# Kernel optimization log

Measured on AMD Instinct MI355X. Metric: run time of the kernel, lower is better.

Reference implementation:

```python
import jax, jax.numpy as jnp
import numpy as np

ROPE_BASE = 10000.0

def _rope_cos_sin(T, d, dtype):
    inv_freq = 1.0 / (ROPE_BASE ** (jnp.arange(0, d, 2, dtype=jnp.float32) / d))
    t = jnp.arange(T, dtype=jnp.float32)
    freqs = t[:, None] * inv_freq[None, :]           # [T, d/2]
    emb = jnp.concatenate([freqs, freqs], axis=-1)   # [T, d]
    return jnp.cos(emb).astype(dtype), jnp.sin(emb).astype(dtype)

def _rotate_half(x):
    x1, x2 = jnp.split(x, 2, axis=-1)
    return jnp.concatenate([-x2, x1], axis=-1)

def setup_inputs() -> dict:
    key = jax.random.key(0)
    k1, k2, k3, k4 = jax.random.split(key, 4)
    B, T, C, H = 4, 4096, 1024, 64
    x = jax.random.normal(k1, (B, T, C), dtype=jnp.float32)
    s = 1.0 / np.sqrt(C)
    Wq = jax.random.normal(k2, (H, C), dtype=jnp.float32) * s
    Wk = jax.random.normal(k3, (H, C), dtype=jnp.float32) * s
    Wv = jax.random.normal(k4, (H, C), dtype=jnp.float32) * s
    return {"x": x, "Wq": Wq, "Wk": Wk, "Wv": Wv}

def reference(x, Wq, Wk, Wv):
    B, T, C = x.shape
    H = Wq.shape[0]
    q = jnp.einsum('btc,hc->bth', x, Wq)
    k = jnp.einsum('btc,hc->bth', x, Wk)
    v = jnp.einsum('btc,hc->bth', x, Wv)
    cos, sin = _rope_cos_sin(T, H, x.dtype)
    q = q * cos + _rotate_half(q) * sin
    k = k * cos + _rotate_half(k) * sin
    # NOTE: original scales by dim_model**-0.5 (C), not head_size
    wei = jnp.einsum('bth,bsh->bts', q, k) * (C ** -0.5)
    causal = jnp.tril(jnp.ones((T, T), dtype=bool))
    wei = jnp.where(causal, wei, -jnp.inf)
    wei = jax.nn.softmax(wei, axis=-1)
    # dropout p=0.0 (identity)
    out = jnp.einsum('bts,bsh->bth', wei, v)
    return out
```

## Files before the change

### kernel.cpp

```cpp
#include <hip/hip_runtime.h>
#include <hip/hip_bf16.h>
#include <math.h>

typedef __attribute__((ext_vector_type(8))) __bf16 bf16x8;
typedef __attribute__((ext_vector_type(4))) float f32x4;
typedef __attribute__((ext_vector_type(16))) float f32x16;
typedef __attribute__((ext_vector_type(4))) float float4_t;
typedef __attribute__((ext_vector_type(4))) unsigned int uint4_t;

#define NB 4
#define TSEQ 4096
#define CD 1024
#define HD 64
#define NCH 32
#define CHT 2

static __device__ __forceinline__ unsigned short f2bf(float f) {
    union { float f; unsigned u; } v; v.f = f;
    unsigned r = v.u + 0x7fffu + ((v.u >> 16) & 1u);
    return (unsigned short)(r >> 16);
}
static __device__ __forceinline__ float bf2f(unsigned short u) {
    union { unsigned int i; float f; } v; v.i = ((unsigned int)u) << 16;
    return v.f;
}
static __device__ __forceinline__ unsigned int pk2(float a, float b) {
    union { __bf16 h[2]; unsigned int u; } x;
    x.h[0] = (__bf16)a; x.h[1] = (__bf16)b;
    return x.u;
}

__global__ __launch_bounds__(256) void wcvt_kernel(const float* __restrict__ wq,
                                                   const float* __restrict__ wk,
                                                   const float* __restrict__ wv,
                                                   unsigned short* __restrict__ wb) {
    int i = blockIdx.x * 256 + threadIdx.x;
    int j = i >> 10;
    int col = i & 1023;
    int jb = j >> 4, off = j & 15;
    int sub = ((jb & 1) << 5) | ((jb & 2) << 3);
    int srcrow = (jb < 8) ? (sub + off) : ((jb - 8) * 16 + off);
    const float* src = (jb < 4) ? wq : ((jb < 8) ? wk : wv);
    wb[i] = f2bf(src[srcrow * 1024 + col]);
}

__global__ __launch_bounds__(256) void qkv_kernel(const float* __restrict__ x,
                                                  const unsigned short* __restrict__ wb,
                                                  unsigned short* __restrict__ qo,
                                                  unsigned short* __restrict__ ko,
                                                  unsigned short* __restrict__ vt) {
    __shared__ unsigned short xs[64][72];
    __shared__ unsigned short ws[64][72];
    const int tid = threadIdx.x;
    const int wave = tid >> 6, lane = tid & 63;
    const int lr = lane & 15;
    const int lk = (lane >> 4) << 3;
    const int rowg = (lane >> 4) << 2;
    const int row0 = blockIdx.x * 64;
    const int cbi = blockIdx.y;
    const int cb = cbi * 64;

    f32x4 acc[4];
#pragma unroll
    for (int i = 0; i < 4; ++i) acc[i] = (f32x4){0.f, 0.f, 0.f, 0.f};

    const int sr = tid >> 2;
    const int sc = (tid & 3) << 4;

    for (int k0 = 0; k0 < CD; k0 += 64) {
        __syncthreads();
        {
            const float4_t* s4 =
                reinterpret_cast<const float4_t*>(x + (size_t)(row0 + sr) * CD + k0 + sc);
            alignas(16) unsigned short tmp[16];
#pragma unroll
            for (int j = 0; j < 4; ++j) {
                float4_t f = s4[j];
#pragma unroll
                for (int e = 0; e < 4; ++e) tmp[j * 4 + e] = f2bf(f[e]);
            }
            *reinterpret_cast<uint4_t*>(&xs[sr][sc]) = *reinterpret_cast<const uint4_t*>(&tmp[0]);
            *reinterpret_cast<uint4_t*>(&xs[sr][sc + 8]) = *reinterpret_cast<const uint4_t*>(&tmp[8]);
        }
        {
            const uint4_t* wsrc =
                reinterpret_cast<const uint4_t*>(wb + (size_t)(cb + sr) * CD + k0 + sc);
            *reinterpret_cast<uint4_t*>(&ws[sr][sc]) = wsrc[0];
            *reinterpret_cast<uint4_t*>(&ws[sr][sc + 8]) = wsrc[1];
        }
        __syncthreads();
#pragma unroll
        for (int kk = 0; kk < 2; ++kk) {
            bf16x8 a = *reinterpret_cast<const bf16x8*>(&xs[wave * 16 + lr][kk * 32 + lk]);
#pragma unroll
            for (int c = 0; c < 4; ++c) {
                bf16x8 bfr = *reinterpret_cast<const bf16x8*>(&ws[c * 16 + lr][kk * 32 + lk]);
                acc[c] = __builtin_amdgcn_mfma_f32_16x16x32_bf16(a, bfr, acc[c], 0, 0, 0);
            }
        }
    }

    const int gr0 = row0 + wave * 16 + rowg;
    const int bidx = gr0 >> 12;
    const int tb = gr0 & (TSEQ - 1);
    if (cbi < 2) {
        unsigned short* o = (cbi == 0) ? qo : ko;
        const float sc2 = (cbi == 0) ? 0.045084218764560315f : 1.0f;
        const float l2b = 0.4152410118609215f;
        const float invf0 = exp2f(-(float)lr * l2b);
        const float invf1 = exp2f(-(float)(lr + 16) * l2b);
#pragma unroll
        for (int r = 0; r < 4; ++r) {
            float t = (float)(tb + r);
            float s0, c0, s1, c1;
            sincosf(t * invf0, &s0, &c0);
            sincosf(t * invf1, &s1, &c1);
            size_t ro = (size_t)(gr0 + r) * HD;
            float lo, hi;
            lo = acc[0][r]; hi = acc[1][r];
            o[ro + 0 + lr]  = f2bf((lo * c0 - hi * s0) * sc2);
            o[ro + 32 + lr] = f2bf((hi * c0 + lo * s0) * sc2);
            lo = acc[2][r]; hi = acc[3][r];
            o[ro + 16 + lr] = f2bf((lo * c1 - hi * s1) * sc2);
            o[ro + 48 + lr] = f2bf((hi * c1 + lo * s1) * sc2);
        }
    } else {
#pragma unroll
        for (int r = 0; r < 4; ++r) {
            size_t vbase = (size_t)bidx * HD * TSEQ + (size_t)(tb + r);
            vt[vbase + (size_t)(0 + lr) * TSEQ]  = f2bf(acc[0][r]);
            vt[vbase + (size_t)(16 + lr) * TSEQ] = f2bf(acc[1][r]);
            vt[vbase + (size_t)(32 + lr) * TSEQ] = f2bf(acc[2][r]);
            vt[vbase + (size_t)(48 + lr) * TSEQ] = f2bf(acc[3][r]);
        }
    }
}

__global__ __launch_bounds__(128, 3) void attn_partial(const unsigned short* __restrict__ q,
                                                       const unsigned short* __restrict__ k,
                                                       const unsigned short* __restrict__ vt,
                                                       unsigned short* __restrict__ po,
                                                       float* __restrict__ pm,
                                                       float* __restrict__ pl) {
    const int chunk = blockIdx.x, b = blockIdx.z;
    const int qt = 63 - blockIdx.y;
    const int kt0 = chunk * CHT;
    if (kt0 > qt) return;
    const int ktend = min(qt, kt0 + CHT - 1);

    __shared__ unsigned short ks[64][72];
    __shared__ unsigned short vs[64][72];
    const int tid = threadIdx.x;
    const int wave = tid >> 6, lane = tid & 63;
    const int l31 = lane & 31;
    const int h = lane >> 5;
    const int h8 = h << 3;
    const int qrow0 = qt * 64 + wave * 32;
    const int qpos = qrow0 + l31;

    const unsigned short* qb_ = q + ((size_t)(b * TSEQ + qpos)) * HD + h8;
    bf16x8 qf[4];
#pragma unroll
    for (int s = 0; s < 4; ++s)
        qf[s] = *reinterpret_cast<const bf16x8*>(qb_ + 16 * s);

    f32x16 oacc[2];
#pragma unroll
    for (int dt = 0; dt < 2; ++dt)
#pragma unroll
        for (int r = 0; r < 16; ++r) oacc[dt][r] = 0.f;
    float mreg = -INFINITY;
    float lsum = 0.f;

    const int srow = tid >> 1;
    const int scol = (tid & 1) << 5;
    const unsigned short* kbase = k + (size_t)b * TSEQ * HD;
    const unsigned short* vbase = vt + (size_t)b * HD * TSEQ;
    uint4_t kr[4], vr[4];
    {
        const int s0l = kt0 * 64;
        const unsigned short* kp = kbase + (size_t)(s0l + srow) * HD + scol;
        const unsigned short* vp = vbase + (size_t)srow * TSEQ + s0l + scol;
#pragma unroll
        for (int j = 0; j < 4; ++j) {
            kr[j] = *reinterpret_cast<const uint4_t*>(kp + 8 * j);
            vr[j] = *reinterpret_cast<const uint4_t*>(vp + 8 * j);
        }
    }

    for (int kt = kt0; kt <= ktend; ++kt) {
        const int s0 = kt * 64;
        __syncthreads();
#pragma unroll
        for (int j = 0; j < 4; ++j) {
            *reinterpret_cast<uint4_t*>(&ks[srow][scol + 8 * j]) = kr[j];
            *reinterpret_cast<uint4_t*>(&vs[srow][scol + 8 * j]) = vr[j];
        }
        __syncthreads();
        if (kt < ktend) {
            const int s0l = s0 + 64;
            const unsigned short* kp = kbase + (size_t)(s0l + srow) * HD + scol;
            const unsigned short* vp = vbase + (size_t)srow * TSEQ + s0l + scol;
#pragma unroll
            for (int j = 0; j < 4; ++j) {
                kr[j] = *reinterpret_cast<const uint4_t*>(kp + 8 * j);
                vr[j] = *reinterpret_cast<const uint4_t*>(vp + 8 * j);
            }
        }

        f32x16 sacc[2];
#pragma unroll
        for (int blk = 0; blk < 2; ++blk)
#pragma unroll
            for (int r = 0; r < 16; ++r) sacc[blk][r] = 0.f;
        __builtin_amdgcn_s_setprio(1);
#pragma unroll
        for (int s = 0; s < 4; ++s) {
            bf16x8 ka = *reinterpret_cast<const bf16x8*>(&ks[l31][16 * s + h8]);
            bf16x8 kb2 = *reinterpret_cast<const bf16x8*>(&ks[32 + l31][16 * s + h8]);
            sacc[0] = __builtin_amdgcn_mfma_f32_32x32x16_bf16(ka, qf[s], sacc[0], 0, 0, 0);
            sacc[1] = __builtin_amdgcn_mfma_f32_32x32x16_bf16(kb2, qf[s], sacc[1], 0, 0, 0);
        }
        __builtin_amdgcn_s_setprio(0);

        if (kt == qt) {
#pragma unroll
            for (int blk = 0; blk < 2; ++blk)
#pragma unroll
                for (int r = 0; r < 16; ++r) {
                    int kvpos = s0 + 32 * blk + (r & 3) + ((r >> 2) << 3) + (h << 2);
                    if (kvpos > qpos) sacc[blk][r] = -INFINITY;
                }
        }

        float tm[8];
#pragma unroll
        for (int r = 0; r < 8; ++r)
            tm[r] = fmaxf(fmaxf(sacc[0][r], sacc[0][r + 8]),
                          fmaxf(sacc[1][r], sacc[1][r + 8]));
#pragma unroll
        for (int r = 0; r < 4; ++r) tm[r] = fmaxf(tm[r], tm[r + 4]);
        float mx = fmaxf(fmaxf(tm[0], tm[1]), fmaxf(tm[2], tm[3]));
        mx = fmaxf(mx, __shfl_xor(mx, 32, 64));

        const bool newmax = !__all(mx <= mreg + 7.0f);
        if (newmax) {
            float mnew = fmaxf(mreg, mx);
            float corr = __builtin_amdgcn_exp2f(mreg - mnew);
            mreg = mnew;
            lsum *= corr;
#pragma unroll
            for (int dt = 0; dt < 2; ++dt)
#pragma unroll
                for (int r = 0; r < 16; ++r) oacc[dt][r] *= corr;
        }

        float pvv[2][16];
#pragma unroll
        for (int blk = 0; blk < 2; ++blk)
#pragma unroll
            for (int r = 0; r < 16; ++r)
                pvv[blk][r] = __builtin_amdgcn_exp2f(sacc[blk][r] - mreg);
        float ts[8];
#pragma unroll
        for (int r = 0; r < 8; ++r)
            ts[r] = (pvv[0][r] + pvv[0][r + 8]) + (pvv[1][r] + pvv[1][r + 8]);
#pragma unroll
        for (int r = 0; r < 4; ++r) ts[r] += ts[r + 4];
        float psum = (ts[0] + ts[1]) + (ts[2] + ts[3]);
        psum += __shfl_xor(psum, 32, 64);
        lsum += psum;

        unsigned int cw[2][4][2];
#pragma unroll
        for (int blk = 0; blk < 2; ++blk)
#pragma unroll
            for (int G = 0; G < 4; ++G) {
                cw[blk][G][0] = pk2(pvv[blk][4 * G], pvv[blk][4 * G + 1]);
                cw[blk][G][1] = pk2(pvv[blk][4 * G + 2], pvv[blk][4 * G + 3]);
            }

        const bool hif = (h == 1);
        __builtin_amdgcn_s_setprio(1);
#pragma unroll
        for (int s = 0; s < 4; ++s) {
            const int blk = s >> 1, base = (s & 1) << 1;
            unsigned int a0 = cw[blk][base][0],     a1 = cw[blk][base][1];
            unsigned int b0 = cw[blk][base + 1][0], b1 = cw[blk][base + 1][1];
            unsigned int s0w = hif ? a0 : b0;
            unsigned int s1w = hif ? a1 : b1;
            unsigned int r0 = __shfl_xor(s0w, 32, 64);
            unsigned int r1 = __shfl_xor(s1w, 32, 64);
            uint4_t pw;
            pw[0] = hif ? r0 : a0;
            pw[1] = hif ? r1 : a1;
            pw[2] = hif ? b0 : r0;
            pw[3] = hif ? b1 : r1;
            bf16x8 pfrag = *reinterpret_cast<const bf16x8*>(&pw);
            bf16x8 v0 = *reinterpret_cast<const bf16x8*>(&vs[l31][16 * s + h8]);
            bf16x8 v1 = *reinterpret_cast<const bf16x8*>(&vs[32 + l31][16 * s + h8]);
            oacc[0] = __builtin_amdgcn_mfma_f32_32x32x16_bf16(v0, pfrag, oacc[0], 0, 0, 0);
            oacc[1] = __builtin_amdgcn_mfma_f32_32x32x16_bf16(v1, pfrag, oacc[1], 0, 0, 0);
        }
        __builtin_amdgcn_s_setprio(0);
    }

    const int slot = (((b << 6) + qt) << 5) + chunk;
    unsigned short* pob = po + (size_t)slot * 4096;
#pragma unroll
    for (int dt = 0; dt < 2; ++dt)
#pragma unroll
        for (int r = 0; r < 16; ++r) {
            int d = 32 * dt + (r & 3) + ((r >> 2) << 3) + (h << 2);
            pob[d * 64 + wave * 32 + l31] = f2bf(oacc[dt][r]);
        }
    if (h == 0) {
        pm[slot * 64 + wave * 32 + l31] = mreg;
        pl[slot * 64 + wave * 32 + l31] = lsum;
    }
}

__global__ __launch_bounds__(256) void attn_combine(const unsigned short* __restrict__ po,
                                                    const float* __restrict__ pm,
                                                    const float* __restrict__ pl,
                                                    float* __restrict__ out) {
    __shared__ float sm[64][17];
    const int bq = blockIdx.x;
    const int dg = blockIdx.y;
    const int qt = bq & 63;
    const int nch = (qt >> 1) + 1;
    const int qi = threadIdx.x & 63;
    const int jj = threadIdx.x >> 6;
    const int sbase = bq << 5;

    float pmv[NCH];
#pragma unroll
    for (int c = 0; c < NCH; ++c)
        pmv[c] = (c < nch) ? pm[(size_t)(sbase + c) * 64 + qi] : -INFINITY;
    float tmv[NCH];
#pragma unroll
    for (int c = 0; c < NCH; ++c) tmv[c] = pmv[c];
#pragma unroll
    for (int s = NCH / 2; s >= 1; s >>= 1)
#pragma unroll
        for (int c = 0; c < NCH / 2; ++c)
            if (c < s) tmv[c] = fmaxf(tmv[c], tmv[c + s]);
    const float M = tmv[0];

    float L = 0.f;
    float a0 = 0.f, a1 = 0.f, a2 = 0.f, a3 = 0.f;
    const int dbase = dg * 16 + jj * 4;
#pragma unroll 4
    for (int c = 0; c < nch; ++c) {
        float w = exp2f(pmv[c] - M);
        L += w * pl[(size_t)(sbase + c) * 64 + qi];
        const unsigned short* p = po + (size_t)(sbase + c) * 4096 + dbase * 64 + qi;
        a0 += w * bf2f(p[0]);
        a1 += w * bf2f(p[64]);
        a2 += w * bf2f(p[128]);
        a3 += w * bf2f(p[192]);
    }
    const float inv = 1.f / L;
    sm[qi][jj * 4 + 0] = a0 * inv;
    sm[qi][jj * 4 + 1] = a1 * inv;
    sm[qi][jj * 4 + 2] = a2 * inv;
    sm[qi][jj * 4 + 3] = a3 * inv;
    __syncthreads();
    const int row = threadIdx.x >> 2;
    const int c4 = (threadIdx.x & 3) << 2;
    float4_t f;
#pragma unroll
    for (int e = 0; e < 4; ++e) f[e] = sm[row][c4 + e];
    *reinterpret_cast<float4_t*>(out + (size_t)bq * 4096 + row * 64 + dg * 16 + c4) = f;
}

extern "C" void kernel_launch(void* const* d_in, const int* in_sizes, int n_in,
                              void* d_out, int out_size, void* d_ws, size_t ws_size,
                              hipStream_t stream) {
    const float* x = (const float*)d_in[0];
    const float* wq = (const float*)d_in[1];
    const float* wk = (const float*)d_in[2];
    const float* wv = (const float*)d_in[3];
    float* out = (float*)d_out;

    unsigned short* wb = (unsigned short*)d_ws;
    unsigned short* qb = wb + 3 * HD * CD;
    unsigned short* kb = qb + (size_t)NB * TSEQ * HD;
    unsigned short* vtb = kb + (size_t)NB * TSEQ * HD;
    unsigned short* pob = vtb + (size_t)NB * TSEQ * HD;
    float* pm = (float*)(pob + (size_t)8192 * 4096);
    float* pl = pm + (size_t)8192 * 64;

    wcvt_kernel<<<768, 256, 0, stream>>>(wq, wk, wv, wb);
    qkv_kernel<<<dim3(256, 3), 256, 0, stream>>>(x, wb, qb, kb, vtb);
    attn_partial<<<dim3(NCH, 64, NB), 128, 0, stream>>>(qb, kb, vtb, pob, pm, pl);
    attn_combine<<<dim3(NB * 64, 4), 256, 0, stream>>>(pob, pm, pl, out);
}
```

Baseline: 76.44 us.

## Widen attention partial blocks to 128 query rows with 4-tile KV chunks

The split-KV attention kernel now uses 256-thread blocks covering 128 query rows (4 waves) instead of 64, and each block processes 4 KV tiles per chunk instead of 2. Each K/V tile staged in shared memory is therefore shared by twice as many query rows, and the number of partial results the combine kernel must merge is halved. The per-wave causal skip and mask condition are generalised, and the running max starts at a large negative finite value so fully masked waves produce no NaN. In exchange, waves whose rows lie above the diagonal idle within a block, and there are fewer, longer blocks, which may leave the GPU less evenly loaded.

```diff
diff --git a/kernel.cpp b/kernel.cpp
--- a/kernel.cpp
+++ b/kernel.cpp
@@ -12,8 +12,9 @@
 #define TSEQ 4096
 #define CD 1024
 #define HD 64
-#define NCH 32
-#define CHT 2
+#define NCH 16
+#define CHT 4
+#define QB 32
 
 static __device__ __forceinline__ unsigned short f2bf(float f) {
     union { float f; unsigned u; } v; v.f = f;
@@ -136,17 +137,17 @@
     }
 }
 
-__global__ __launch_bounds__(128, 3) void attn_partial(const unsigned short* __restrict__ q,
+__global__ __launch_bounds__(256, 4) void attn_partial(const unsigned short* __restrict__ q,
                                                        const unsigned short* __restrict__ k,
                                                        const unsigned short* __restrict__ vt,
                                                        unsigned short* __restrict__ po,
                                                        float* __restrict__ pm,
                                                        float* __restrict__ pl) {
-    const int chunk = blockIdx.x, b = blockIdx.z;
-    const int qt = 63 - blockIdx.y;
+    const int chunk = blockIdx.x, qb = blockIdx.y, b = blockIdx.z;
+    const int ktend_blk = 2 * qb + 1;
     const int kt0 = chunk * CHT;
-    if (kt0 > qt) return;
-    const int ktend = min(qt, kt0 + CHT - 1);
+    if (kt0 > ktend_blk) return;
+    const int ktend = min(ktend_blk, kt0 + CHT - 1);
 
     __shared__ unsigned short ks[64][72];
     __shared__ unsigned short vs[64][72];
@@ -155,7 +156,7 @@
     const int l31 = lane & 31;
     const int h = lane >> 5;
     const int h8 = h << 3;
-    const int qrow0 = qt * 64 + wave * 32;
+    const int qrow0 = qb * 128 + wave * 32;
     const int qpos = qrow0 + l31;
 
     const unsigned short* qb_ = q + ((size_t)(b * TSEQ + qpos)) * HD + h8;
@@ -169,44 +170,38 @@
     for (int dt = 0; dt < 2; ++dt)
 #pragma unroll
         for (int r = 0; r < 16; ++r) oacc[dt][r] = 0.f;
-    float mreg = -INFINITY;
+    float mreg = -1.0e30f;
     float lsum = 0.f;
 
-    const int srow = tid >> 1;
-    const int scol = (tid & 1) << 5;
+    const int srow = tid >> 2;
+    const int scol = (tid & 3) << 4;
     const unsigned short* kbase = k + (size_t)b * TSEQ * HD;
     const unsigned short* vbase = vt + (size_t)b * HD * TSEQ;
-    uint4_t kr[4], vr[4];
-    {
-        const int s0l = kt0 * 64;
+    uint4_t kr[2], vr[2];
+
+    auto loadtile = [&](int kt) {
+        const int s0l = kt * 64;
         const unsigned short* kp = kbase + (size_t)(s0l + srow) * HD + scol;
         const unsigned short* vp = vbase + (size_t)srow * TSEQ + s0l + scol;
-#pragma unroll
-        for (int j = 0; j < 4; ++j) {
-            kr[j] = *reinterpret_cast<const uint4_t*>(kp + 8 * j);
-            vr[j] = *reinterpret_cast<const uint4_t*>(vp + 8 * j);
-        }
-    }
+        kr[0] = *reinterpret_cast<const uint4_t*>(kp);
+        kr[1] = *reinterpret_cast<const uint4_t*>(kp + 8);
+        vr[0] = *reinterpret_cast<const uint4_t*>(vp);
+        vr[1] = *reinterpret_cast<const uint4_t*>(vp + 8);
+    };
+
+    loadtile(kt0);
 
     for (int kt = kt0; kt <= ktend; ++kt) {
         const int s0 = kt * 64;
         __syncthreads();
-#pragma unroll
-        for (int j = 0; j < 4; ++j) {
-            *reinterpret_cast<uint4_t*>(&ks[srow][scol + 8 * j]) = kr[j];
-            *reinterpret_cast<uint4_t*>(&vs[srow][scol + 8 * j]) = vr[j];
-        }
+        *reinterpret_cast<uint4_t*>(&ks[srow][scol]) = kr[0];
+        *reinterpret_cast<uint4_t*>(&ks[srow][scol + 8]) = kr[1];
+        *reinterpret_cast<uint4_t*>(&vs[srow][scol]) = vr[0];
+        *reinterpret_cast<uint4_t*>(&vs[srow][scol + 8]) = vr[1];
         __syncthreads();
-        if (kt < ktend) {
-            const int s0l = s0 + 64;
-            const unsigned short* kp = kbase + (size_t)(s0l + srow) * HD + scol;
-            const unsigned short* vp = vbase + (size_t)srow * TSEQ + s0l + scol;
-#pragma unroll
-            for (int j = 0; j < 4; ++j) {
-                kr[j] = *reinterpret_cast<const uint4_t*>(kp + 8 * j);
-                vr[j] = *reinterpret_cast<const uint4_t*>(vp + 8 * j);
-            }
-        }
+        if (kt < ktend) loadtile(kt + 1);
+
+        if (s0 > qrow0 + 31) continue;
 
         f32x16 sacc[2];
 #pragma unroll
@@ -223,7 +218,7 @@
         }
         __builtin_amdgcn_s_setprio(0);
 
-        if (kt == qt) {
+        if (s0 + 63 > qrow0) {
 #pragma unroll
             for (int blk = 0; blk < 2; ++blk)
 #pragma unroll
@@ -305,18 +300,18 @@
         __builtin_amdgcn_s_setprio(0);
     }
 
-    const int slot = (((b << 6) + qt) << 5) + chunk;
-    unsigned short* pob = po + (size_t)slot * 4096;
+    const int slot = (((b << 5) + qb) << 4) + chunk;
+    unsigned short* pob = po + (size_t)slot * 8192;
 #pragma unroll
     for (int dt = 0; dt < 2; ++dt)
 #pragma unroll
         for (int r = 0; r < 16; ++r) {
             int d = 32 * dt + (r & 3) + ((r >> 2) << 3) + (h << 2);
-            pob[d * 64 + wave * 32 + l31] = f2bf(oacc[dt][r]);
+            pob[d * 128 + wave * 32 + l31] = f2bf(oacc[dt][r]);
         }
     if (h == 0) {
-        pm[slot * 64 + wave * 32 + l31] = mreg;
-        pl[slot * 64 + wave * 32 + l31] = lsum;
+        pm[slot * 128 + wave * 32 + l31] = mreg;
+        pl[slot * 128 + wave * 32 + l31] = lsum;
     }
 }
 
@@ -328,15 +323,18 @@
     const int bq = blockIdx.x;
     const int dg = blockIdx.y;
     const int qt = bq & 63;
-    const int nch = (qt >> 1) + 1;
+    const int b = bq >> 6;
+    const int qb = qt >> 1, half = qt & 1;
+    const int nch = (qb >> 1) + 1;
     const int qi = threadIdx.x & 63;
     const int jj = threadIdx.x >> 6;
-    const int sbase = bq << 5;
+    const int slotb = (((b << 5) + qb) << 4);
+    const int qoff = half * 64 + qi;
 
     float pmv[NCH];
 #pragma unroll
     for (int c = 0; c < NCH; ++c)
-        pmv[c] = (c < nch) ? pm[(size_t)(sbase + c) * 64 + qi] : -INFINITY;
+        pmv[c] = (c < nch) ? pm[(size_t)(slotb + c) * 128 + qoff] : -1.0e30f;
     float tmv[NCH];
 #pragma unroll
     for (int c = 0; c < NCH; ++c) tmv[c] = pmv[c];
@@ -353,12 +351,12 @@
 #pragma unroll 4
     for (int c = 0; c < nch; ++c) {
         float w = exp2f(pmv[c] - M);
-        L += w * pl[(size_t)(sbase + c) * 64 + qi];
-        const unsigned short* p = po + (size_t)(sbase + c) * 4096 + dbase * 64 + qi;
+        L += w * pl[(size_t)(slotb + c) * 128 + qoff];
+        const unsigned short* p = po + (size_t)(slotb + c) * 8192 + dbase * 128 + qoff;
         a0 += w * bf2f(p[0]);
-        a1 += w * bf2f(p[64]);
-        a2 += w * bf2f(p[128]);
-        a3 += w * bf2f(p[192]);
+        a1 += w * bf2f(p[128]);
+        a2 += w * bf2f(p[256]);
+        a3 += w * bf2f(p[384]);
     }
     const float inv = 1.f / L;
     sm[qi][jj * 4 + 0] = a0 * inv;
@@ -388,11 +386,11 @@
     unsigned short* kb = qb + (size_t)NB * TSEQ * HD;
     unsigned short* vtb = kb + (size_t)NB * TSEQ * HD;
     unsigned short* pob = vtb + (size_t)NB * TSEQ * HD;
-    float* pm = (float*)(pob + (size_t)8192 * 4096);
-    float* pl = pm + (size_t)8192 * 64;
+    float* pm = (float*)(pob + (size_t)2048 * 8192);
+    float* pl = pm + (size_t)2048 * 128;
 
     wcvt_kernel<<<768, 256, 0, stream>>>(wq, wk, wv, wb);
     qkv_kernel<<<dim3(256, 3), 256, 0, stream>>>(x, wb, qb, kb, vtb);
-    attn_partial<<<dim3(NCH, 64, NB), 128, 0, stream>>>(qb, kb, vtb, pob, pm, pl);
+    attn_partial<<<dim3(NCH, QB, NB), 256, 0, stream>>>(qb, kb, vtb, pob, pm, pl);
     attn_combine<<<dim3(NB * 64, 4), 256, 0, stream>>>(pob, pm, pl, out);
 }
```

New measurement: 63.29 us. 1.21x faster.
